# Kernel tuning notes

Measured on AMD Instinct MI355X. Metric: run time of the kernel, lower is better.

The kernel has to match this reference:

```python
import jax, jax.numpy as jnp
import numpy as np

TOPK = 5
DUP_THRESH = 0.9999  # scores >= this are treated as 'self' matches and masked out
EPS = 1e-12


def _l2norm(x):
    n = jnp.sqrt(jnp.sum(x * x, axis=-1, keepdims=True))
    return x / jnp.maximum(n, EPS)


def setup_inputs() -> dict:
    key = jax.random.key(0)
    k1, k2 = jax.random.split(key)
    query_embeddings = jax.random.normal(k1, (4096, 128), dtype=jnp.float32)
    user_embeddings = jax.random.normal(k2, (100000, 128), dtype=jnp.float32)
    return {"query_embeddings": query_embeddings, "user_embeddings": user_embeddings}


def reference(query_embeddings, user_embeddings):
    # Module normalizes the stored table at load time and the queries per call.
    ue = _l2norm(user_embeddings)                      # [N, D]
    q = _l2norm(query_embeddings)                      # [B, D]
    sims = jnp.matmul(q, ue.T)                         # [B, N]

    k1 = min(TOPK + 1, sims.shape[-1])
    topk_values, topk_indices = jax.lax.top_k(sims, k1)  # [B, k1]

    # Vectorized version of the per-row mask / gather / pad loop:
    # keep candidates with score < 0.9999, take first TOPK of them,
    # pad with the last valid candidate; if none valid, fall back to raw top-k.
    mask = topk_values < DUP_THRESH                    # [B, k1]
    n_valid = jnp.sum(mask.astype(jnp.int32), axis=-1)  # [B]
    # stable argsort puts valid positions first, preserving score order
    order = jnp.argsort((~mask).astype(jnp.int32), axis=-1, stable=True)  # [B, k1]

    j = jnp.arange(TOPK)[None, :]                      # [1, TOPK]
    # position within `order`: clamp to last valid slot (padding-with-last behavior)
    pos_in_order = jnp.minimum(j, jnp.maximum(n_valid[:, None] - 1, 0))
    pos_valid = jnp.take_along_axis(order, pos_in_order, axis=-1)  # [B, TOPK]
    # fallback when no valid candidates: first TOPK raw positions
    pos = jnp.where(n_valid[:, None] > 0, pos_valid, j)            # [B, TOPK]

    sel_indices = jnp.take_along_axis(topk_indices, pos, axis=-1)  # [B, TOPK]
    similarity_scores = jnp.take_along_axis(topk_values, pos, axis=-1)  # [B, TOPK]
    similar_embeddings = ue[sel_indices]               # [B, TOPK, D]
    return similar_embeddings, similarity_scores
```

## Files before the change

### kernel.cpp

```cpp
#include <hip/hip_runtime.h>
#include <hip/hip_bf16.h>
#include <stdint.h>

#define D 128
#define TOPK 5
#define K1 6
#define CAP 128
#define TAU 0.30f
#define DUP 0.9999f
#define USPLIT 16
#define GSTR 64

typedef float f32x16 __attribute__((ext_vector_type(16)));
typedef int i32x8 __attribute__((ext_vector_type(8)));
typedef unsigned char uchar;
typedef unsigned int u32;

static __device__ __forceinline__ ushort f2fp8x2(float a, float b) {
#if __has_builtin(__builtin_amdgcn_cvt_pk_fp8_f32)
    int w = __builtin_amdgcn_cvt_pk_fp8_f32(a, b, 0, false);
    return (ushort)(w & 0xFFFF);
#else
    auto enc = [](float x) -> uchar {
        uint32_t u = __builtin_bit_cast(uint32_t, x);
        uchar s = (uchar)((u >> 24) & 0x80u);
        float ax = fabsf(x);
        if (ax < 0.0078125f) return s;
        if (ax > 448.f) return (uchar)(s | 0x7E);
        uint32_t au = u & 0x7FFFFFFFu;
        uint32_t r = au + 0x0007FFFFu + ((au >> 20) & 1u);
        int e8 = (int)(r >> 23) - 127 + 7;
        uint32_t m = (r >> 20) & 7u;
        if (e8 <= 0) { uint32_t full = (8u | m) >> (1 - e8); return (uchar)(s | full); }
        return (uchar)(s | ((uint32_t)e8 << 3) | m);
    };
    return (ushort)(enc(a) | ((ushort)enc(b) << 8));
#endif
}

__global__ __launch_bounds__(256) void k_norm_users(const float* __restrict__ u,
        uchar* __restrict__ ub8, float* __restrict__ uinv, int nu) {
    __shared__ __align__(16) uchar tile[4096];
    const int g = blockIdx.x;
    const int wv = threadIdx.x >> 6, lane = threadIdx.x & 63;
    #pragma unroll
    for (int rr = 0; rr < 8; rr++) {
        int r32 = wv * 8 + rr;
        int row = g * 32 + r32;
        size_t loff = (size_t)(lane >> 4) * 1024 + r32 * 32 + ((lane << 1) & 31);
        if (row < nu) {
            float2 v = ((const float2*)(u + (size_t)row * D))[lane];
            float s = v.x * v.x + v.y * v.y;
            #pragma unroll
            for (int o = 32; o; o >>= 1) s += __shfl_xor(s, o);
            float inv = 1.0f / fmaxf(sqrtf(s), 1e-12f);
            *(ushort*)(tile + loff) = f2fp8x2(v.x * inv, v.y * inv);
            if (lane == 0) uinv[row] = inv;
        } else {
            *(ushort*)(tile + loff) = 0;
            if (lane == 0) uinv[row] = 0.f;
        }
    }
    __syncthreads();
    ((uint4*)(ub8 + (size_t)g * 4096))[threadIdx.x] = ((const uint4*)tile)[threadIdx.x];
}

__global__ __launch_bounds__(256) void k_norm_queries(const float* __restrict__ q,
        uchar* __restrict__ qf8, float* __restrict__ qn, int nq) {
    int row = blockIdx.x * 4 + (threadIdx.x >> 6);
    int lane = threadIdx.x & 63;
    if (row >= nq) return;
    float2 v = ((const float2*)(q + (size_t)row * D))[lane];
    float s = v.x * v.x + v.y * v.y;
    #pragma unroll
    for (int o = 32; o; o >>= 1) s += __shfl_xor(s, o);
    float inv = 1.0f / fmaxf(sqrtf(s), 1e-12f);
    float2 w; w.x = v.x * inv; w.y = v.y * inv;
    ((float2*)(qn + (size_t)row * D))[lane] = w;
    size_t off = (size_t)(row >> 5) * 4096 + (size_t)(lane >> 4) * 1024
               + (row & 31) * 32 + ((lane << 1) & 31);
    *(ushort*)(qf8 + off) = f2fp8x2(w.x, w.y);
}

__global__ __launch_bounds__(256, 2) void k_gemm_filter(
        const uchar* __restrict__ ub8, const uchar* __restrict__ qf8,
        int* __restrict__ cnt, int* __restrict__ cand,
        int ngroup, int nu) {
    __shared__ __align__(16) uchar Bl[4 * 4096];
    const int tid = threadIdx.x;
    const int wv = tid >> 6, lane = tid & 63;
    const int half = lane >> 5, l31 = lane & 31;
    const int us = blockIdx.x % USPLIT;
    const int qt = blockIdx.x / USPLIT;
    const int qbase = qt * 128;
    const int ws = us * 4 + wv;

    {
        const uint4* src = (const uint4*)(qf8 + (size_t)qt * 16384);
        uint4* dst = (uint4*)Bl;
        #pragma unroll
        for (int i = 0; i < 4; i++) dst[tid + i * 256] = src[tid + i * 256];
    }
    __syncthreads();

    const uchar* ap0 = ub8 + (size_t)half * 1024 + (size_t)l31 * 32;
    const uchar* bp0 = Bl + (size_t)half * 1024 + (size_t)l31 * 32;

    #define LOADA(dst_, gg) do {                                              \
        const uchar* ap_ = ap0 + (size_t)(gg) * 4096;                         \
        dst_[0] = *(const i32x8*)(ap_);                                       \
        dst_[1] = *(const i32x8*)(ap_ + 2048);                                \
    } while (0)

    #define BODY(aa, gg) do {                                                 \
        f32x16 acc[4];                                                        \
        _Pragma("unroll")                                                     \
        for (int n = 0; n < 4; n++)                                           \
            _Pragma("unroll")                                                 \
            for (int i2 = 0; i2 < 16; i2++) acc[n][i2] = 0.f;                 \
        _Pragma("unroll")                                                     \
        for (int m = 0; m < 2; m++) {                                         \
            _Pragma("unroll")                                                 \
            for (int n = 0; n < 4; n++) {                                     \
                i32x8 bf = *(const i32x8*)(bp0 + n * 4096 + m * 2048);        \
                acc[n] = __builtin_amdgcn_mfma_scale_f32_32x32x64_f8f6f4(     \
                    aa[m], bf, acc[n], 0, 0,                                  \
                    0, 0x7F7F7F7F, 0, 0x7F7F7F7F);                            \
            }                                                                 \
        }                                                                     \
        const int ub0_ = (gg) * 32 + half * 4;                                \
        _Pragma("unroll")                                                     \
        for (int n = 0; n < 4; n++) {                                         \
            float t0 = fmaxf(fmaxf(acc[n][0], acc[n][1]), fmaxf(acc[n][2], acc[n][3])); \
            float t1 = fmaxf(fmaxf(acc[n][4], acc[n][5]), fmaxf(acc[n][6], acc[n][7])); \
            float t2 = fmaxf(fmaxf(acc[n][8], acc[n][9]), fmaxf(acc[n][10], acc[n][11])); \
            float t3 = fmaxf(fmaxf(acc[n][12], acc[n][13]), fmaxf(acc[n][14], acc[n][15])); \
            float m0 = fmaxf(fmaxf(t0, t1), fmaxf(t2, t3));                   \
            if (m0 > TAU) {                                                   \
                int qq = qbase + n * 32 + l31;                                \
                _Pragma("unroll")                                             \
                for (int rg = 0; rg < 16; rg++) {                             \
                    float s0 = acc[n][rg];                                    \
                    if (s0 > TAU) {                                           \
                        int urow = ub0_ + (rg & 3) + 8 * (rg >> 2);           \
                        if (urow < nu) {                                      \
                            int pos = atomicAdd(&cnt[qq], 1);                 \
                            if (pos < CAP) cand[qq * CAP + pos] = urow;       \
                        }                                                     \
                    }                                                         \
                }                                                             \
            }                                                                 \
        }                                                                     \
    } while (0)

    i32x8 a0[2], a1[2];
    int g = ws;
    if (g < ngroup) {
        LOADA(a0, g);
        for (; g + GSTR < ngroup; g += 2 * GSTR) {
            LOADA(a1, g + GSTR);
            BODY(a0, g);
            if (g + 2 * GSTR < ngroup) LOADA(a0, g + 2 * GSTR);
            BODY(a1, g + GSTR);
        }
        if (g < ngroup) BODY(a0, g);
    }
    #undef LOADA
    #undef BODY
}

__global__ __launch_bounds__(256) void k_rescore(
        const float* __restrict__ users, const float* __restrict__ qn,
        const float* __restrict__ uinv,
        const int* __restrict__ cnt, const int* __restrict__ cand,
        float* __restrict__ out_emb, float* __restrict__ out_sc) {
    __shared__ float s_sc[CAP];
    __shared__ int s_id[CAP];
    __shared__ float s_outv[TOPK];
    __shared__ int s_outi[TOPK];
    int q = blockIdx.x;
    int tid = threadIdx.x, wv = tid >> 6, lane = tid & 63;
    int c = cnt[q]; c = c < CAP ? c : CAP;
    for (int j = tid; j < CAP; j += 256) { s_sc[j] = -1e30f; s_id[j] = 0; }
    __syncthreads();
    float2 qv = ((const float2*)(qn + (size_t)q * D))[lane];
    for (int j = wv; j < c; j += 4) {
        int u = cand[q * CAP + j];
        float2 uv = ((const float2*)(users + (size_t)u * D))[lane];
        float qu = qv.x * uv.x + qv.y * uv.y;
        #pragma unroll
        for (int o = 32; o; o >>= 1) qu += __shfl_xor(qu, o);
        if (lane == 0) { s_sc[j] = qu * uinv[u]; s_id[j] = u; }
    }
    __syncthreads();

    if (wv == 0) {
        float c0 = s_sc[lane], c1 = s_sc[lane + 64];
        bool u0 = false, u1 = false;
        float topv[K1]; int tops[K1];
        for (int k = 0; k < K1; k++) {
            float v0 = u0 ? -1e30f : c0;
            float v1 = u1 ? -1e30f : c1;
            float v = fmaxf(v0, v1);
            int sl = (v1 > v0) ? lane + 64 : lane;
            #pragma unroll
            for (int o = 32; o; o >>= 1) {
                float ov = __shfl_xor(v, o);
                int os = __shfl_xor(sl, o);
                if (ov > v || (ov == v && os < sl)) { v = ov; sl = os; }
            }
            topv[k] = v; tops[k] = sl;
            u0 = u0 || (sl == lane);
            u1 = u1 || (sl == lane + 64);
        }
        int vk[K1]; int nv = 0;
        #pragma unroll
        for (int k = 0; k < K1; k++) { if (topv[k] < DUP) { vk[nv] = k; nv++; } }
        if (lane < TOPK) {
            int j = lane; int k;
            if (nv > 0) { int p = (j < nv - 1) ? j : (nv - 1); k = vk[p]; }
            else k = j;
            s_outi[j] = tops[k];
            s_outv[j] = topv[k];
        }
    }
    __syncthreads();
    for (int j = wv; j < TOPK; j += 4) {
        int sl = s_outi[j];
        int u = s_id[sl];
        float rn = uinv[u];
        float2 uv = ((const float2*)(users + (size_t)u * D))[lane];
        float2 o; o.x = uv.x * rn; o.y = uv.y * rn;
        ((float2*)(out_emb + ((size_t)q * TOPK + j) * D))[lane] = o;
        if (lane == 0) out_sc[q * TOPK + j] = s_outv[j];
    }
}

extern "C" void kernel_launch(void* const* d_in, const int* in_sizes, int n_in,
                              void* d_out, int out_size, void* d_ws, size_t ws_size,
                              hipStream_t stream) {
    const float* q = (const float*)d_in[0];
    const float* u = (const float*)d_in[1];
    int nq = in_sizes[0] / D;
    int nu = in_sizes[1] / D;
    int nchunk = (nu + 127) / 128;
    int npad = nchunk * 128;
    int ngroup = npad / 32;

    char* ws = (char*)d_ws;
    uchar* ub8 = (uchar*)ws;                        size_t o1 = (size_t)npad * D;
    uchar* qf8 = (uchar*)(ws + o1);                 size_t o2 = o1 + (size_t)nq * D;
    float* qn  = (float*)(ws + o2);                 size_t o3 = o2 + (size_t)nq * D * 4;
    float* uinv = (float*)(ws + o3);                size_t o4 = o3 + (size_t)npad * 4;
    int*   cnt = (int*)(ws + o4);                   size_t o5 = o4 + (size_t)nq * 4;
    int*   cand = (int*)(ws + o5);

    float* out_emb = (float*)d_out;
    float* out_sc = out_emb + (size_t)nq * TOPK * D;

    hipMemsetAsync(cnt, 0, (size_t)nq * 4, stream);
    k_norm_users<<<ngroup, 256, 0, stream>>>(u, ub8, uinv, nu);
    k_norm_queries<<<(nq + 3) / 4, 256, 0, stream>>>(q, qf8, qn, nq);
    k_gemm_filter<<<(nq / 128) * USPLIT, 256, 0, stream>>>(ub8, qf8, cnt, cand, ngroup, nu);
    k_rescore<<<nq, 256, 0, stream>>>(u, qn, uinv, cnt, cand, out_emb, out_sc);
}
```

Before: 223.0 us.

## Split query fp8 LDS layout into 16-byte halves, raise occupancy and user split

Changes the fp8 query tile layout so each lane's 32-byte B fragment is stored as two 16-byte chunks 512 bytes apart. The intent is to reduce LDS bank conflicts when lanes read their B fragments. It also raises launch bounds to 3 blocks per CU, increases the user split from 16 to 24, and seeds the first MFMA with a zero constant instead of explicitly zeroing the accumulators. The higher occupancy target may force register spills, and the wider split adds more blocks, each reloading the query tile.

```diff
diff --git a/kernel.cpp b/kernel.cpp
--- a/kernel.cpp
+++ b/kernel.cpp
@@ -8,11 +8,12 @@
 #define CAP 128
 #define TAU 0.30f
 #define DUP 0.9999f
-#define USPLIT 16
-#define GSTR 64
+#define USPLIT 24
+#define GSTR 96
 
 typedef float f32x16 __attribute__((ext_vector_type(16)));
 typedef int i32x8 __attribute__((ext_vector_type(8)));
+typedef int i32x4 __attribute__((ext_vector_type(4)));
 typedef unsigned char uchar;
 typedef unsigned int u32;
 
@@ -77,12 +78,14 @@
     float inv = 1.0f / fmaxf(sqrtf(s), 1e-12f);
     float2 w; w.x = v.x * inv; w.y = v.y * inv;
     ((float2*)(qn + (size_t)row * D))[lane] = w;
-    size_t off = (size_t)(row >> 5) * 4096 + (size_t)(lane >> 4) * 1024
-               + (row & 31) * 32 + ((lane << 1) & 31);
+    int col = lane << 1;
+    int j = col & 31;
+    size_t off = (size_t)(row >> 5) * 4096 + (size_t)(col >> 5) * 1024
+               + (size_t)(j >> 4) * 512 + (row & 31) * 16 + (j & 15);
     *(ushort*)(qf8 + off) = f2fp8x2(w.x, w.y);
 }
 
-__global__ __launch_bounds__(256, 2) void k_gemm_filter(
+__global__ __launch_bounds__(256, 3) void k_gemm_filter(
         const uchar* __restrict__ ub8, const uchar* __restrict__ qf8,
         int* __restrict__ cnt, int* __restrict__ cand,
         int ngroup, int nu) {
@@ -104,7 +107,10 @@
     __syncthreads();
 
     const uchar* ap0 = ub8 + (size_t)half * 1024 + (size_t)l31 * 32;
-    const uchar* bp0 = Bl + (size_t)half * 1024 + (size_t)l31 * 32;
+    const uchar* bp0 = Bl + (size_t)half * 1024 + (size_t)l31 * 16;
+
+    const f32x16 z16 = {0.f, 0.f, 0.f, 0.f, 0.f, 0.f, 0.f, 0.f,
+                        0.f, 0.f, 0.f, 0.f, 0.f, 0.f, 0.f, 0.f};
 
     #define LOADA(dst_, gg) do {                                              \
         const uchar* ap_ = ap0 + (size_t)(gg) * 4096;                         \
@@ -112,21 +118,27 @@
         dst_[1] = *(const i32x8*)(ap_ + 2048);                                \
     } while (0)
 
+    #define LOADB(bf_, n_, m_) do {                                           \
+        const uchar* bp_ = bp0 + (n_) * 4096 + (m_) * 2048;                   \
+        i32x4 lo_ = *(const i32x4*)bp_;                                       \
+        i32x4 hi_ = *(const i32x4*)(bp_ + 512);                               \
+        bf_[0] = lo_[0]; bf_[1] = lo_[1]; bf_[2] = lo_[2]; bf_[3] = lo_[3];   \
+        bf_[4] = hi_[0]; bf_[5] = hi_[1]; bf_[6] = hi_[2]; bf_[7] = hi_[3];   \
+    } while (0)
+
     #define BODY(aa, gg) do {                                                 \
         f32x16 acc[4];                                                        \
         _Pragma("unroll")                                                     \
-        for (int n = 0; n < 4; n++)                                           \
-            _Pragma("unroll")                                                 \
-            for (int i2 = 0; i2 < 16; i2++) acc[n][i2] = 0.f;                 \
+        for (int n = 0; n < 4; n++) {                                         \
+            i32x8 bf; LOADB(bf, n, 0);                                        \
+            acc[n] = __builtin_amdgcn_mfma_scale_f32_32x32x64_f8f6f4(         \
+                aa[0], bf, z16, 0, 0, 0, 0x7F7F7F7F, 0, 0x7F7F7F7F);          \
+        }                                                                     \
         _Pragma("unroll")                                                     \
-        for (int m = 0; m < 2; m++) {                                         \
-            _Pragma("unroll")                                                 \
-            for (int n = 0; n < 4; n++) {                                     \
-                i32x8 bf = *(const i32x8*)(bp0 + n * 4096 + m * 2048);        \
-                acc[n] = __builtin_amdgcn_mfma_scale_f32_32x32x64_f8f6f4(     \
-                    aa[m], bf, acc[n], 0, 0,                                  \
-                    0, 0x7F7F7F7F, 0, 0x7F7F7F7F);                            \
-            }                                                                 \
+        for (int n = 0; n < 4; n++) {                                         \
+            i32x8 bf; LOADB(bf, n, 1);                                        \
+            acc[n] = __builtin_amdgcn_mfma_scale_f32_32x32x64_f8f6f4(         \
+                aa[1], bf, acc[n], 0, 0, 0, 0x7F7F7F7F, 0, 0x7F7F7F7F);       \
         }                                                                     \
         const int ub0_ = (gg) * 32 + half * 4;                                \
         _Pragma("unroll")                                                     \
@@ -166,6 +178,7 @@
         if (g < ngroup) BODY(a0, g);
     }
     #undef LOADA
+    #undef LOADB
     #undef BODY
 }
 
```

After: 208.2 us. 6.6% less time.
